# Kernel optimization log

Hardware: AMD Instinct MI355X
Metric: run time of the kernel (lower is better)

The kernel has to match this reference:

```python
import jax, jax.numpy as jnp
import numpy as np

N, B, D, T = 128, 512, 128, 16  # regions, batch, embed_dim, decode steps
C_CLIP = 10.0                   # tanh_clipping
NEG = -1e9


def setup_inputs() -> dict:
    key = jax.random.key(0)
    ks = jax.random.split(key, 40)
    s = 1.0 / np.sqrt(D)

    def w(k, shape):
        return jax.random.uniform(k, shape, jnp.float32, -s, s)

    return {
        'data': jax.random.normal(ks[0], (N, B, 4), jnp.float32),
        'node_embed': w(ks[1], (4, D)),
        'init_placeholder': w(ks[2], (D,)),
        'W1_w': w(ks[3], (D, D)), 'W1_b': w(ks[4], (D,)),
        'W2_w': w(ks[5], (D, D)), 'W2_b': w(ks[6], (D,)),
        'W3_w': w(ks[7], (D, D)), 'W3_b': w(ks[8], (D,)),
        'agg1_w': w(ks[9], (D, D)), 'agg1_b': w(ks[10], (D,)),
        'agg2_w': w(ks[11], (D, D)), 'agg2_b': w(ks[12], (D,)),
        'agg3_w': w(ks[13], (D, D)), 'agg3_b': w(ks[14], (D,)),
        'r1': jnp.ones((1,), jnp.float32),
        'r2': jnp.ones((1,), jnp.float32),
        'r3': jnp.ones((1,), jnp.float32),
        'lstm_Wih': w(ks[15], (4 * D, D)), 'lstm_Whh': w(ks[16], (4 * D, D)),
        'lstm_bih': w(ks[17], (4 * D,)), 'lstm_bhh': w(ks[18], (4 * D,)),
        'ptr_Wq': w(ks[19], (D, D)), 'ptr_bq': w(ks[20], (D,)),
        'ptr_Wref': w(ks[21], (D, D)), 'ptr_bref': w(ks[22], (D,)),
        'ptr_v': w(ks[23], (D,)),
        'glm_Wq': w(ks[24], (D, D)), 'glm_bq': w(ks[25], (D,)),
        'glm_Wref': w(ks[26], (D, D)), 'glm_bref': w(ks[27], (D,)),
        'glm_v': w(ks[28], (D,)),
    }


def _lin(x, w, b):
    return x @ w.T + b


def _attn_logits(q, e, Wq, bq, v):
    # q: [B,D], e: [B,D,N] (1x1-conv-projected ref). Bahdanau: v . tanh(Wq q + e)
    qq = (q @ Wq.T + bq)[:, :, None]          # [B,D,1]
    return jnp.einsum('d,bdn->bn', v, jnp.tanh(qq + e))  # [B,N]


def reference(data, node_embed, init_placeholder,
              W1_w, W1_b, W2_w, W2_b, W3_w, W3_b,
              agg1_w, agg1_b, agg2_w, agg2_b, agg3_w, agg3_b,
              r1, r2, r3,
              lstm_Wih, lstm_Whh, lstm_bih, lstm_bhh,
              ptr_Wq, ptr_bq, ptr_Wref, ptr_bref, ptr_v,
              glm_Wq, glm_bq, glm_Wref, glm_bref, glm_v):
    # node embedding: [N,B,4] @ [4,D] -> [N,B,D]
    emb = jnp.einsum('nbf,fd->nbd', data, node_embed)
    # GPN graph context: gated local transform + aggregated mean over nodes
    ctx = r1 * _lin(emb, W1_w, W1_b) + (1.0 - r1) * jax.nn.relu(_lin(emb.mean(0), agg1_w, agg1_b))
    ctx = r2 * _lin(ctx, W2_w, W2_b) + (1.0 - r2) * jax.nn.relu(_lin(ctx.mean(0), agg2_w, agg2_b))
    ctx = r3 * _lin(ctx, W3_w, W3_b) + (1.0 - r3) * jax.nn.relu(_lin(ctx.mean(0), agg3_w, agg3_b))
    # precompute 1x1-conv ref projections (ref is fixed over decode steps): [B,D,N]
    e_ptr = jnp.einsum('oi,nbi->bon', ptr_Wref, ctx) + ptr_bref[None, :, None]
    e_glm = jnp.einsum('oi,nbi->bon', glm_Wref, ctx) + glm_bref[None, :, None]
    emb_bnd = emb.transpose(1, 0, 2)  # [B,N,D] for gathering next decoder input

    def step(carry, _):
        h, c, x, visited = carry
        # LSTMCell (torch gate order i,f,g,o)
        gates = x @ lstm_Wih.T + lstm_bih + h @ lstm_Whh.T + lstm_bhh
        i, f, g, o = jnp.split(gates, 4, axis=-1)
        c = jax.nn.sigmoid(f) * c + jax.nn.sigmoid(i) * jnp.tanh(g)
        h = jax.nn.sigmoid(o) * jnp.tanh(c)
        # one glimpse (use_tanh=False), masked
        lg = _attn_logits(h, e_glm, glm_Wq, glm_bq, glm_v)
        lg = jnp.where(visited, NEG, lg)
        gl = jnp.einsum('bdn,bn->bd', e_glm, jax.nn.softmax(lg, axis=-1))
        # pointer (use_tanh=True, C=10), masked
        lp = C_CLIP * jnp.tanh(_attn_logits(gl, e_ptr, ptr_Wq, ptr_bq, ptr_v))
        lp = jnp.where(visited, NEG, lp)
        log_p = jax.nn.log_softmax(lp, axis=-1)  # temp = 1.0
        sel = jnp.argmax(log_p, axis=-1)         # greedy decode, [B]
        visited = visited | jax.nn.one_hot(sel, N, dtype=bool)
        x = jnp.take_along_axis(emb_bnd, sel[:, None, None], axis=1)[:, 0]  # [B,D]
        return (h, c, x, visited), log_p

    h0 = jnp.zeros((B, D), emb.dtype)
    c0 = jnp.zeros((B, D), emb.dtype)
    x0 = jnp.broadcast_to(init_placeholder, (B, D)).astype(emb.dtype)
    visited0 = jnp.zeros((B, N), bool)
    _, log_ps = jax.lax.scan(step, (h0, c0, x0, visited0), None, length=T)
    return log_ps  # [T,B,N]
```

## Files before the change

### kernel.cpp

```cpp
#include <hip/hip_runtime.h>
#include <math.h>


#define NREG   128
#define BATCH  512
#define DIM    128
#define TSTEPS 16
#define NEGV   (-1e9f)
#define LOG2E  1.4426950408889634f

__device__ __forceinline__ float fexp2(float x) { return __builtin_amdgcn_exp2f(x); }
__device__ __forceinline__ float frcp(float x)  { return __builtin_amdgcn_rcpf(x); }
__device__ __forceinline__ float fast_tanh(float x) {
    return 1.f - 2.f * frcp(1.f + fexp2(2.8853900817779268f * x));
}
__device__ __forceinline__ float fast_sig(float x) {
    return frcp(1.f + fexp2(-LOG2E * x));
}
__device__ __forceinline__ float fast_exp(float x) { return fexp2(LOG2E * x); }
__device__ __forceinline__ float fast_log(float x) {
    return __builtin_amdgcn_logf(x) * 0.6931471805599453f;
}

__device__ __forceinline__ float dot128(const float* __restrict__ wrow,
                                        const float* __restrict__ s) {
    float a0 = 0.f, a1 = 0.f, a2 = 0.f, a3 = 0.f;
#pragma unroll
    for (int k = 0; k < 128; k += 4) {
        a0 += wrow[k] * s[k];     a1 += wrow[k + 1] * s[k + 1];
        a2 += wrow[k + 2] * s[k + 2]; a3 += wrow[k + 3] * s[k + 3];
    }
    return (a0 + a1) + (a2 + a3);
}

__global__ __launch_bounds__(256) void k_misc(
    const float* __restrict__ Whh, const float* __restrict__ gWq,
    const float* __restrict__ Wih, const float* __restrict__ NE,
    const float* __restrict__ init_ph,
    const float* __restrict__ bih, const float* __restrict__ bhh,
    const float* __restrict__ W1, const float* __restrict__ W2,
    const float* __restrict__ r1p, const float* __restrict__ r2p,
    const float* __restrict__ data,
    float* __restrict__ WhhT, float* __restrict__ gWqT,
    float* __restrict__ WihNE4, float* __restrict__ g0,
    float* __restrict__ bc, float* __restrict__ A21, float* __restrict__ md)
{
    int blk = blockIdx.x, t = threadIdx.x;
    if (blk < 64) {
        int idx = blk * 256 + t;
        int g = idx >> 5, k0 = (idx & 31) * 4;
        float4 v = *(const float4*)(Whh + g * 128 + k0);
        WhhT[(k0 + 0) * 512 + g] = v.x;
        WhhT[(k0 + 1) * 512 + g] = v.y;
        WhhT[(k0 + 2) * 512 + g] = v.z;
        WhhT[(k0 + 3) * 512 + g] = v.w;
    } else if (blk < 80) {
        int idx = (blk - 64) * 256 + t;
        int o = idx >> 5, i0 = (idx & 31) * 4;
        float4 v = *(const float4*)(gWq + o * 128 + i0);
        gWqT[(i0 + 0) * 128 + o] = v.x;
        gWqT[(i0 + 1) * 128 + o] = v.y;
        gWqT[(i0 + 2) * 128 + o] = v.z;
        gWqT[(i0 + 3) * 128 + o] = v.w;
    } else if (blk < 82) {
        int g = (blk - 80) * 256 + t;
        float a0 = 0.f, a1 = 0.f, a2 = 0.f, a3 = 0.f;
        for (int d = 0; d < 128; d += 4) {
            float4 wv = *(const float4*)(Wih + g * 128 + d);
            float4 n0 = *(const float4*)(NE + 0 * 128 + d);
            float4 n1 = *(const float4*)(NE + 1 * 128 + d);
            float4 n2 = *(const float4*)(NE + 2 * 128 + d);
            float4 n3 = *(const float4*)(NE + 3 * 128 + d);
            a0 += wv.x * n0.x + wv.y * n0.y + wv.z * n0.z + wv.w * n0.w;
            a1 += wv.x * n1.x + wv.y * n1.y + wv.z * n1.z + wv.w * n1.w;
            a2 += wv.x * n2.x + wv.y * n2.y + wv.z * n2.z + wv.w * n2.w;
            a3 += wv.x * n3.x + wv.y * n3.y + wv.z * n3.z + wv.w * n3.w;
        }
        *(float4*)(WihNE4 + g * 4) = make_float4(a0, a1, a2, a3);
    } else if (blk == 82) {
        for (int g = t; g < 512; g += 256) {
            float acc = 0.f;
            for (int d = 0; d < 128; d += 4) {
                float4 wv = *(const float4*)(Wih + g * 128 + d);
                float4 iv = *(const float4*)(init_ph + d);
                acc += wv.x * iv.x + wv.y * iv.y + wv.z * iv.z + wv.w * iv.w;
            }
            g0[g] = acc;
            bc[g] = bih[g] + bhh[g];
        }
    } else if (blk < 147) {
        int r = blk - 83;
        int o = r * 2 + (t >> 7), i = t & 127;
        float acc = 0.f;
        for (int k = 0; k < 128; k++) acc += W2[o * 128 + k] * W1[k * 128 + i];
        A21[o * 128 + i] = r1p[0] * r2p[0] * acc;
    } else {
        int idx = (blk - 147) * 256 + t;
        float acc = 0.f;
        for (int n = 0; n < 128; n++) acc += data[n * 2048 + idx];
        md[idx] = acc * (1.f / 128.f);
    }
}

__global__ __launch_bounds__(256) void k_mm2(const float* __restrict__ W3,
                                             const float* __restrict__ A21,
                                             const float* __restrict__ r3p,
                                             float* __restrict__ A3) {
    int o = blockIdx.x * 2 + (threadIdx.x >> 7), i = threadIdx.x & 127;
    float acc = 0.f;
    for (int k = 0; k < 128; k++) acc += W3[o * 128 + k] * A21[k * 128 + i];
    A3[o * 128 + i] = r3p[0] * acc;
}

__global__ __launch_bounds__(256) void k_mm3(const float* __restrict__ gWr,
                                             const float* __restrict__ pWr,
                                             const float* __restrict__ A3,
                                             float* __restrict__ Mg,
                                             float* __restrict__ Mp) {
    int blk = blockIdx.x;
    const float* W = (blk < 64) ? gWr : pWr;
    float* Out = (blk < 64) ? Mg : Mp;
    int r = blk & 63;
    int o = r * 2 + (threadIdx.x >> 7), i = threadIdx.x & 127;
    float acc = 0.f;
    for (int k = 0; k < 128; k++) acc += W[o * 128 + k] * A3[k * 128 + i];
    Out[o * 128 + i] = acc;
}

__global__ __launch_bounds__(256) void k_small2(const float* __restrict__ NE,
                                                const float* __restrict__ Mg,
                                                const float* __restrict__ Mp,
                                                float* __restrict__ Qg4,
                                                float* __restrict__ Qp4) {
    const float* M = (blockIdx.x == 0) ? Mg : Mp;
    float* Q = (blockIdx.x == 0) ? Qg4 : Qp4;
    int t = threadIdx.x;
    for (int idx = t; idx < 512; idx += 256) {
        int o = idx >> 2, f = idx & 3;
        float acc = 0.f;
        for (int d = 0; d < 128; d++) acc += NE[f * 128 + d] * M[o * 128 + d];
        Q[idx] = acc;
    }
}

__global__ __launch_bounds__(256) void k_small3(const float* __restrict__ pWq,
                                                const float* __restrict__ Qg4,
                                                float* __restrict__ GPQ4) {
    int t = threadIdx.x;
    for (int idx = t; idx < 512; idx += 256) {
        int o = idx >> 2, f = idx & 3;
        float acc = 0.f;
        for (int i = 0; i < 128; i++) acc += pWq[o * 128 + i] * Qg4[i * 4 + f];
        GPQ4[idx] = acc;
    }
}

__global__ __launch_bounds__(256) void k_perb(
    const float* __restrict__ md, const float* __restrict__ NE,
    const float* __restrict__ a1w, const float* __restrict__ a1b,
    const float* __restrict__ a2w, const float* __restrict__ a2b,
    const float* __restrict__ a3w, const float* __restrict__ a3b,
    const float* __restrict__ W1, const float* __restrict__ b1,
    const float* __restrict__ W2, const float* __restrict__ b2,
    const float* __restrict__ W3, const float* __restrict__ b3,
    const float* __restrict__ gWr, const float* __restrict__ gbr,
    const float* __restrict__ pWr, const float* __restrict__ pbr,
    const float* __restrict__ pWq, const float* __restrict__ pbq,
    const float* __restrict__ r1p, const float* __restrict__ r2p,
    const float* __restrict__ r3p,
    float* __restrict__ og, float* __restrict__ op, float* __restrict__ pog)
{
    __shared__ float Ws[128 * 129];
    __shared__ float me[1024], Cv[1024], Mv[1024], Tv[1024], C2[1024], M2[1024];
    __shared__ float NEs[512], mdS[32];
    const int t = threadIdx.x;
    const int b0 = blockIdx.x * 8;
    const float r1 = r1p[0], r2 = r2p[0], r3 = r3p[0];

#define STAGE_W(Wptr)                                                          \
    for (int i = t * 4; i < 16384; i += 1024) {                                \
        float4 v = *(const float4*)((Wptr) + i);                               \
        int oo = i >> 7, kk = i & 127;                                         \
        float* p = &Ws[oo * 129 + kk];                                         \
        p[0] = v.x; p[1] = v.y; p[2] = v.z; p[3] = v.w;                        \
    }

    if (t < 32) mdS[t] = md[b0 * 4 + t];
    for (int i = t; i < 512; i += 256) NEs[i] = NE[i];
    __syncthreads();
    for (int idx = t; idx < 1024; idx += 256) {
        int j = idx >> 7, d = idx & 127;
        me[idx] = mdS[j * 4 + 0] * NEs[d] + mdS[j * 4 + 1] * NEs[128 + d] +
                  mdS[j * 4 + 2] * NEs[256 + d] + mdS[j * 4 + 3] * NEs[384 + d];
    }
    STAGE_W(a1w);
    __syncthreads();
    {
        int o = t & 127, jg = t >> 7;
        for (int jj = 0; jj < 4; jj++) {
            int j = jg * 4 + jj;
            float acc = dot128(&Ws[o * 129], &me[j * 128]);
            Tv[j * 128 + o] = (1.f - r1) * fmaxf(acc + a1b[o], 0.f);
        }
    }
    __syncthreads();
    STAGE_W(W1);
    for (int idx = t; idx < 1024; idx += 256) Cv[idx] = r1 * b1[idx & 127] + Tv[idx];
    __syncthreads();
    {
        int o = t & 127, jg = t >> 7;
        for (int jj = 0; jj < 4; jj++) {
            int j = jg * 4 + jj;
            float acc = dot128(&Ws[o * 129], &me[j * 128]);
            Mv[j * 128 + o] = r1 * (acc + b1[o]) + Tv[j * 128 + o];
        }
    }
    __syncthreads();
    STAGE_W(a2w);
    __syncthreads();
    {
        int o = t & 127, jg = t >> 7;
        for (int jj = 0; jj < 4; jj++) {
            int j = jg * 4 + jj;
            float acc = dot128(&Ws[o * 129], &Mv[j * 128]);
            Tv[j * 128 + o] = (1.f - r2) * fmaxf(acc + a2b[o], 0.f);
        }
    }
    __syncthreads();
    STAGE_W(W2);
    __syncthreads();
    {
        int o = t & 127, jg = t >> 7;
        for (int jj = 0; jj < 4; jj++) {
            int j = jg * 4 + jj;
            float ac = dot128(&Ws[o * 129], &Cv[j * 128]);
            float am = dot128(&Ws[o * 129], &Mv[j * 128]);
            C2[j * 128 + o] = r2 * (ac + b2[o]) + Tv[j * 128 + o];
            M2[j * 128 + o] = r2 * (am + b2[o]) + Tv[j * 128 + o];
        }
    }
    __syncthreads();
    STAGE_W(a3w);
    __syncthreads();
    {
        int o = t & 127, jg = t >> 7;
        for (int jj = 0; jj < 4; jj++) {
            int j = jg * 4 + jj;
            float acc = dot128(&Ws[o * 129], &M2[j * 128]);
            Tv[j * 128 + o] = (1.f - r3) * fmaxf(acc + a3b[o], 0.f);
        }
    }
    __syncthreads();
    STAGE_W(W3);
    __syncthreads();
    {
        int o = t & 127, jg = t >> 7;
        for (int jj = 0; jj < 4; jj++) {
            int j = jg * 4 + jj;
            float acc = dot128(&Ws[o * 129], &C2[j * 128]);
            Cv[j * 128 + o] = r3 * (acc + b3[o]) + Tv[j * 128 + o];
        }
    }
    __syncthreads();
    STAGE_W(gWr);
    __syncthreads();
    {
        int o = t & 127, jg = t >> 7;
        for (int jj = 0; jj < 4; jj++) {
            int j = jg * 4 + jj;
            float acc = dot128(&Ws[o * 129], &Cv[j * 128]) + gbr[o];
            Mv[j * 128 + o] = acc;
            og[(long)(b0 + j) * 128 + o] = acc;
        }
    }
    __syncthreads();
    STAGE_W(pWr);
    __syncthreads();
    {
        int o = t & 127, jg = t >> 7;
        for (int jj = 0; jj < 4; jj++) {
            int j = jg * 4 + jj;
            op[(long)(b0 + j) * 128 + o] = dot128(&Ws[o * 129], &Cv[j * 128]) + pbr[o];
        }
    }
    __syncthreads();
    STAGE_W(pWq);
    __syncthreads();
    {
        int o = t & 127, jg = t >> 7;
        for (int jj = 0; jj < 4; jj++) {
            int j = jg * 4 + jj;
            pog[(long)(b0 + j) * 128 + o] = dot128(&Ws[o * 129], &Mv[j * 128]) + pbq[o];
        }
    }
#undef STAGE_W
}

__global__ __launch_bounds__(256, 2) void k_decode(
    const float* __restrict__ dataIn,
    const float* __restrict__ WhhT,
    const float* __restrict__ gWqT,
    const float* __restrict__ WihNE4,
    const float* __restrict__ g0,
    const float* __restrict__ bc,
    const float* __restrict__ Qg4, const float* __restrict__ Qp4,
    const float* __restrict__ GPQ4,
    const float* __restrict__ ogG, const float* __restrict__ opG,
    const float* __restrict__ pogG,
    const float* __restrict__ gbq, const float* __restrict__ vgG,
    const float* __restrict__ vpG,
    float* __restrict__ out)
{
    __shared__ float4 dataS[128];
    __shared__ float4 WihS[512];
    __shared__ float4 QgS[128], QpS[128], GPQS[128];
    __shared__ float g0S[512], bcS[512], gatesS[512];
    __shared__ float ogS[128], opS[128], pogS[128], gbqS[128], vgS[128], vpS[128];
    __shared__ float hS[128], cS[128], qpart[2][128], lpart[2][128], qpS[128];
    __shared__ int visitedS[128];
    __shared__ int selS;

    const int t = threadIdx.x;
    const int b = blockIdx.x;

    if (t < 128) {
        dataS[t] = *(const float4*)(dataIn + ((long)t * 512 + b) * 4);
        QgS[t]  = *(const float4*)(Qg4 + t * 4);
        QpS[t]  = *(const float4*)(Qp4 + t * 4);
        GPQS[t] = *(const float4*)(GPQ4 + t * 4);
        ogS[t]  = ogG[(long)b * 128 + t];
        opS[t]  = opG[(long)b * 128 + t];
        pogS[t] = pogG[(long)b * 128 + t];
        gbqS[t] = gbq[t];
        vgS[t]  = vgG[t];
        vpS[t]  = vpG[t];
        hS[t] = 0.f; cS[t] = 0.f;
        visitedS[t] = 0;
    }
    WihS[t] = *(const float4*)(WihNE4 + t * 4);
    WihS[t + 256] = *(const float4*)(WihNE4 + (t + 256) * 4);
    g0S[t] = g0[t]; g0S[t + 256] = g0[t + 256];
    bcS[t] = bc[t]; bcS[t + 256] = bc[t + 256];
    __syncthreads();

    for (int step = 0; step < TSTEPS; step++) {
        {
            float accA, accB;
            if (step == 0) {
                accA = g0S[2 * t]; accB = g0S[2 * t + 1];
            } else {
                float4 xd = dataS[selS];
                float4 wA = WihS[2 * t], wB = WihS[2 * t + 1];
                accA = xd.x * wA.x + xd.y * wA.y + xd.z * wA.z + xd.w * wA.w;
                accB = xd.x * wB.x + xd.y * wB.y + xd.z * wB.z + xd.w * wB.w;
            }
            accA += bcS[2 * t]; accB += bcS[2 * t + 1];
            const float* w = WhhT + 2 * t;
            float a0 = 0.f, a1 = 0.f, b0_ = 0.f, b1_ = 0.f;
#pragma unroll 8
            for (int k = 0; k < 128; k += 2) {
                float2 w0 = *(const float2*)(w + (long)k * 512);
                float2 w1 = *(const float2*)(w + (long)(k + 1) * 512);
                float h0 = hS[k], h1 = hS[k + 1];
                a0 += w0.x * h0; a1 += w0.y * h0;
                b0_ += w1.x * h1; b1_ += w1.y * h1;
            }
            gatesS[2 * t] = accA + a0 + b0_;
            gatesS[2 * t + 1] = accB + a1 + b1_;
        }
        __syncthreads();
        if (t < 128) {
            float ig = fast_sig(gatesS[t]);
            float fg = fast_sig(gatesS[128 + t]);
            float gg = fast_tanh(gatesS[256 + t]);
            float og_ = fast_sig(gatesS[384 + t]);
            float cn = fg * cS[t] + ig * gg;
            cS[t] = cn;
            hS[t] = og_ * fast_tanh(cn);
        }
        __syncthreads();
        {
            int o = t & 127, h2 = t >> 7;
            const float* w = gWqT + (h2 * 64) * 128 + o;
            float a0 = (h2 == 0) ? gbqS[o] : 0.f, a1 = 0.f;
#pragma unroll 8
            for (int i = 0; i < 64; i += 2) {
                a0 += w[i * 128] * hS[h2 * 64 + i];
                a1 += w[(i + 1) * 128] * hS[h2 * 64 + i + 1];
            }
            qpart[h2][o] = a0 + a1;
        }
        __syncthreads();
        {
            int n = t & 127, h2 = t >> 7;
            float4 dn = dataS[n];
            float acc = 0.f;
#pragma unroll 4
            for (int j = 0; j < 64; j++) {
                int d = h2 * 64 + j;
                float4 qg = QgS[d];
                float eg = dn.x * qg.x + dn.y * qg.y + dn.z * qg.z + dn.w * qg.w
                         + ogS[d];
                float q = qpart[0][d] + qpart[1][d];
                acc += vgS[d] * fast_tanh(q + eg);
            }
            lpart[h2][n] = acc;
        }
        __syncthreads();
        if (t < 64) {
            float l0 = visitedS[t]      ? NEGV : lpart[0][t] + lpart[1][t];
            float l1 = visitedS[t + 64] ? NEGV : lpart[0][t + 64] + lpart[1][t + 64];
            float m = fmaxf(l0, l1);
            for (int off = 32; off; off >>= 1) m = fmaxf(m, __shfl_xor(m, off, 64));
            float p0 = fast_exp(l0 - m), p1 = fast_exp(l1 - m);
            float s = p0 + p1;
            float4 d0 = dataS[t], d1 = dataS[t + 64];
            float q0 = p0 * d0.x + p1 * d1.x;
            float q1 = p0 * d0.y + p1 * d1.y;
            float q2 = p0 * d0.z + p1 * d1.z;
            float q3 = p0 * d0.w + p1 * d1.w;
            for (int off = 32; off; off >>= 1) {
                s  += __shfl_xor(s, off, 64);
                q0 += __shfl_xor(q0, off, 64);
                q1 += __shfl_xor(q1, off, 64);
                q2 += __shfl_xor(q2, off, 64);
                q3 += __shfl_xor(q3, off, 64);
            }
            float inv = frcp(s);
            q0 *= inv; q1 *= inv; q2 *= inv; q3 *= inv;
            float4 gA = GPQS[t];
            qpS[t] = q0 * gA.x + q1 * gA.y + q2 * gA.z + q3 * gA.w + pogS[t];
            float4 gB = GPQS[t + 64];
            qpS[t + 64] = q0 * gB.x + q1 * gB.y + q2 * gB.z + q3 * gB.w + pogS[t + 64];
        }
        __syncthreads();
        {
            int n = t & 127, h2 = t >> 7;
            float4 dn = dataS[n];
            float acc = 0.f;
#pragma unroll 4
            for (int j = 0; j < 64; j++) {
                int d = h2 * 64 + j;
                float4 qp = QpS[d];
                float ep = dn.x * qp.x + dn.y * qp.y + dn.z * qp.z + dn.w * qp.w
                         + opS[d];
                acc += vpS[d] * fast_tanh(qpS[d] + ep);
            }
            lpart[h2][n] = acc;
        }
        __syncthreads();
        if (t < 64) {
            float s0 = lpart[0][t] + lpart[1][t];
            float s1 = lpart[0][t + 64] + lpart[1][t + 64];
            float l0 = visitedS[t]      ? NEGV : 10.f * fast_tanh(s0);
            float l1 = visitedS[t + 64] ? NEGV : 10.f * fast_tanh(s1);
            float m = fmaxf(l0, l1);
            for (int off = 32; off; off >>= 1) m = fmaxf(m, __shfl_xor(m, off, 64));
            float p0 = fast_exp(l0 - m), p1 = fast_exp(l1 - m);
            float s = p0 + p1;
            for (int off = 32; off; off >>= 1) s += __shfl_xor(s, off, 64);
            float lse = m + fast_log(s);
            float* outp = out + ((long)step * BATCH + b) * NREG;
            outp[t] = l0 - lse;
            outp[t + 64] = l1 - lse;
            float v; int idx;
            if (l1 > l0) { v = l1; idx = t + 64; } else { v = l0; idx = t; }
            for (int off = 32; off; off >>= 1) {
                float ov = __shfl_xor(v, off, 64);
                int   oi = __shfl_xor(idx, off, 64);
                if (ov > v || (ov == v && oi < idx)) { v = ov; idx = oi; }
            }
            if (t == 0) { selS = idx; visitedS[idx] = 1; }
        }
        __syncthreads();
    }
}

extern "C" void kernel_launch(void* const* d_in, const int* in_sizes, int n_in,
                              void* d_out, int out_size, void* d_ws, size_t ws_size,
                              hipStream_t stream) {
    const float* data = (const float*)d_in[0];
    const float* NE   = (const float*)d_in[1];
    const float* init = (const float*)d_in[2];
    const float* W1w = (const float*)d_in[3];  const float* W1b = (const float*)d_in[4];
    const float* W2w = (const float*)d_in[5];  const float* W2b = (const float*)d_in[6];
    const float* W3w = (const float*)d_in[7];  const float* W3b = (const float*)d_in[8];
    const float* A1w = (const float*)d_in[9];  const float* A1b = (const float*)d_in[10];
    const float* A2w = (const float*)d_in[11]; const float* A2b = (const float*)d_in[12];
    const float* A3w = (const float*)d_in[13]; const float* A3b = (const float*)d_in[14];
    const float* r1  = (const float*)d_in[15];
    const float* r2  = (const float*)d_in[16];
    const float* r3  = (const float*)d_in[17];
    const float* Wih = (const float*)d_in[18]; const float* Whh = (const float*)d_in[19];
    const float* bih = (const float*)d_in[20]; const float* bhh = (const float*)d_in[21];
    const float* pWq = (const float*)d_in[22]; const float* pbq = (const float*)d_in[23];
    const float* pWr = (const float*)d_in[24]; const float* pbr = (const float*)d_in[25];
    const float* pv  = (const float*)d_in[26];
    const float* gWq = (const float*)d_in[27]; const float* gbq = (const float*)d_in[28];
    const float* gWr = (const float*)d_in[29]; const float* gbr = (const float*)d_in[30];
    const float* gv  = (const float*)d_in[31];
    float* out = (float*)d_out;

    float* ws     = (float*)d_ws;
    float* WhhT   = ws;
    float* gWqT   = WhhT + 65536;
    float* WihNE4 = gWqT + 16384;
    float* g0     = WihNE4 + 2048;
    float* bc     = g0 + 512;
    float* A21    = bc + 512;
    float* A3     = A21 + 16384;
    float* Mg     = A3 + 16384;
    float* Mp     = Mg + 16384;
    float* Qg4    = Mp + 16384;
    float* Qp4    = Qg4 + 512;
    float* GPQ4   = Qp4 + 512;
    float* md     = GPQ4 + 512;
    float* og     = md + 2048;
    float* op     = og + 65536;
    float* pog    = op + 65536;

    k_misc<<<155, 256, 0, stream>>>(Whh, gWq, Wih, NE, init, bih, bhh,
                                    W1w, W2w, r1, r2, data,
                                    WhhT, gWqT, WihNE4, g0, bc, A21, md);
    k_mm2<<<64, 256, 0, stream>>>(W3w, A21, r3, A3);
    k_mm3<<<128, 256, 0, stream>>>(gWr, pWr, A3, Mg, Mp);
    k_small2<<<2, 256, 0, stream>>>(NE, Mg, Mp, Qg4, Qp4);
    k_small3<<<1, 256, 0, stream>>>(pWq, Qg4, GPQ4);
    k_perb<<<64, 256, 0, stream>>>(md, NE, A1w, A1b, A2w, A2b, A3w, A3b,
                                   W1w, W1b, W2w, W2b, W3w, W3b,
                                   gWr, gbr, pWr, pbr, pWq, pbq,
                                   r1, r2, r3, og, op, pog);
    k_decode<<<BATCH, 256, 0, stream>>>(data, WhhT, gWqT, WihNE4, g0, bc,
                                        Qg4, Qp4, GPQ4, og, op, pog,
                                        gbq, gv, pv, out);
}
```

Before: 448.8 us.

## Fuse all precompute kernels into one launch and widen decode to 512 threads

Merges the chain of small setup kernels (the weight-product matmuls, Q projections and per-batch GPN context) into a single multi-role k_misc launch. Block 83 computes the low-rank Q vectors by propagating the node embedding through the weight chain, and the other blocks run the per-batch context including the data mean. Weight transposes become float4-packed layouts. The decode kernel runs with 512 threads, splits the attention reduction four ways, and folds the tanh constant and v-sum into precomputed terms so each logit uses one exp2 and one rcp. This removes several launches and serialized small kernels, at the cost of a more complex kernel with heavy LDS use in one launch.

```diff
diff --git a/kernel.cpp b/kernel.cpp
--- a/kernel.cpp
+++ b/kernel.cpp
@@ -8,11 +8,12 @@
 #define TSTEPS 16
 #define NEGV   (-1e9f)
 #define LOG2E  1.4426950408889634f
+#define CT     2.8853900817779268f
 
 __device__ __forceinline__ float fexp2(float x) { return __builtin_amdgcn_exp2f(x); }
 __device__ __forceinline__ float frcp(float x)  { return __builtin_amdgcn_rcpf(x); }
 __device__ __forceinline__ float fast_tanh(float x) {
-    return 1.f - 2.f * frcp(1.f + fexp2(2.8853900817779268f * x));
+    return 1.f - 2.f * frcp(1.f + fexp2(CT * x));
 }
 __device__ __forceinline__ float fast_sig(float x) {
     return frcp(1.f + fexp2(-LOG2E * x));
@@ -27,7 +28,7 @@
     float a0 = 0.f, a1 = 0.f, a2 = 0.f, a3 = 0.f;
 #pragma unroll
     for (int k = 0; k < 128; k += 4) {
-        a0 += wrow[k] * s[k];     a1 += wrow[k + 1] * s[k + 1];
+        a0 += wrow[k] * s[k];         a1 += wrow[k + 1] * s[k + 1];
         a2 += wrow[k + 2] * s[k + 2]; a3 += wrow[k + 3] * s[k + 3];
     }
     return (a0 + a1) + (a2 + a3);
@@ -38,30 +39,41 @@
     const float* __restrict__ Wih, const float* __restrict__ NE,
     const float* __restrict__ init_ph,
     const float* __restrict__ bih, const float* __restrict__ bhh,
-    const float* __restrict__ W1, const float* __restrict__ W2,
+    const float* __restrict__ W1, const float* __restrict__ b1,
+    const float* __restrict__ W2, const float* __restrict__ b2,
+    const float* __restrict__ W3, const float* __restrict__ b3,
+    const float* __restrict__ a1w, const float* __restrict__ a1b,
+    const float* __restrict__ a2w, const float* __restrict__ a2b,
+    const float* __restrict__ a3w, const float* __restrict__ a3b,
+    const float* __restrict__ gWr, const float* __restrict__ gbr,
+    const float* __restrict__ pWr, const float* __restrict__ pbr,
+    const float* __restrict__ pWq, const float* __restrict__ pbq,
     const float* __restrict__ r1p, const float* __restrict__ r2p,
-    const float* __restrict__ data,
-    float* __restrict__ WhhT, float* __restrict__ gWqT,
+    const float* __restrict__ r3p,
+    const float* __restrict__ pv, const float* __restrict__ data,
+    float* __restrict__ WhhP, float* __restrict__ gWqP,
     float* __restrict__ WihNE4, float* __restrict__ g0,
-    float* __restrict__ bc, float* __restrict__ A21, float* __restrict__ md)
+    float* __restrict__ bc, float* __restrict__ sumvp,
+    float* __restrict__ Qgc, float* __restrict__ Qpc, float* __restrict__ GPQ,
+    float* __restrict__ og, float* __restrict__ op, float* __restrict__ pog)
 {
-    int blk = blockIdx.x, t = threadIdx.x;
+    __shared__ float Ws[128 * 129];
+    __shared__ float me[1024], Cv[1024], Mv[1024], Tv[1024], C2[1024], M2[1024];
+    __shared__ float NEs[512], mdS[32];
+    __shared__ float4 Uc[128], Vc[128], Qgu[128];
+
+    const int blk = blockIdx.x, t = threadIdx.x;
+
     if (blk < 64) {
         int idx = blk * 256 + t;
-        int g = idx >> 5, k0 = (idx & 31) * 4;
-        float4 v = *(const float4*)(Whh + g * 128 + k0);
-        WhhT[(k0 + 0) * 512 + g] = v.x;
-        WhhT[(k0 + 1) * 512 + g] = v.y;
-        WhhT[(k0 + 2) * 512 + g] = v.z;
-        WhhT[(k0 + 3) * 512 + g] = v.w;
+        int kb = idx >> 9, g = idx & 511;
+        float4 v = *(const float4*)(Whh + g * 128 + kb * 4);
+        ((float4*)WhhP)[kb * 512 + g] = v;
     } else if (blk < 80) {
         int idx = (blk - 64) * 256 + t;
-        int o = idx >> 5, i0 = (idx & 31) * 4;
-        float4 v = *(const float4*)(gWq + o * 128 + i0);
-        gWqT[(i0 + 0) * 128 + o] = v.x;
-        gWqT[(i0 + 1) * 128 + o] = v.y;
-        gWqT[(i0 + 2) * 128 + o] = v.z;
-        gWqT[(i0 + 3) * 128 + o] = v.w;
+        int ib = idx >> 7, o = idx & 127;
+        float4 v = *(const float4*)(gWq + o * 128 + ib * 4);
+        ((float4*)gWqP)[ib * 128 + o] = v;
     } else if (blk < 82) {
         int g = (blk - 80) * 256 + t;
         float a0 = 0.f, a1 = 0.f, a2 = 0.f, a3 = 0.f;
@@ -88,337 +100,291 @@
             g0[g] = acc;
             bc[g] = bih[g] + bhh[g];
         }
-    } else if (blk < 147) {
-        int r = blk - 83;
-        int o = r * 2 + (t >> 7), i = t & 127;
-        float acc = 0.f;
-        for (int k = 0; k < 128; k++) acc += W2[o * 128 + k] * W1[k * 128 + i];
-        A21[o * 128 + i] = r1p[0] * r2p[0] * acc;
+        if (t < 64) {
+            float sv = pv[t] + pv[t + 64];
+            for (int off = 32; off; off >>= 1) sv += __shfl_xor(sv, off, 64);
+            if (t == 0) sumvp[0] = sv;
+        }
+    } else if (blk == 83) {
+        if (t < 128)
+            Uc[t] = make_float4(NE[t], NE[128 + t], NE[256 + t], NE[384 + t]);
+        __syncthreads();
+#define CH_STAGE(Wp, SRC, DST, SC)                                             \
+        if (t < 128) {                                                         \
+            const float* wr = (Wp) + t * 128;                                  \
+            float ax = 0.f, ay = 0.f, az = 0.f, aw = 0.f;                      \
+            _Pragma("unroll 8")                                                \
+            for (int k = 0; k < 128; k++) {                                    \
+                float w = wr[k]; float4 u = SRC[k];                            \
+                ax += w * u.x; ay += w * u.y; az += w * u.z; aw += w * u.w;    \
+            }                                                                  \
+            float sc = (SC);                                                   \
+            DST[t] = make_float4(sc * ax, sc * ay, sc * az, sc * aw);          \
+        }                                                                      \
+        __syncthreads();
+        CH_STAGE(W1, Uc, Vc, r1p[0])
+        CH_STAGE(W2, Vc, Uc, r2p[0])
+        CH_STAGE(W3, Uc, Vc, r3p[0])
+        CH_STAGE(gWr, Vc, Qgu, 1.f)
+        CH_STAGE(pWr, Vc, Uc, 1.f)
+        CH_STAGE(pWq, Qgu, Vc, 1.f)
+        if (t < 128) {
+            float4 qg = Qgu[t], qp = Uc[t];
+            ((float4*)Qgc)[t] = make_float4(CT * qg.x, CT * qg.y, CT * qg.z, CT * qg.w);
+            ((float4*)Qpc)[t] = make_float4(CT * qp.x, CT * qp.y, CT * qp.z, CT * qp.w);
+            ((float4*)GPQ)[t] = Vc[t];
+        }
+#undef CH_STAGE
     } else {
-        int idx = (blk - 147) * 256 + t;
-        float acc = 0.f;
-        for (int n = 0; n < 128; n++) acc += data[n * 2048 + idx];
-        md[idx] = acc * (1.f / 128.f);
+        const int b0 = (blk - 84) * 8;
+        const float r1 = r1p[0], r2 = r2p[0], r3 = r3p[0];
+#define STAGE_W(Wptr)                                                          \
+        for (int i = t * 4; i < 16384; i += 1024) {                            \
+            float4 v = *(const float4*)((Wptr) + i);                           \
+            int oo = i >> 7, kk = i & 127;                                     \
+            float* p = &Ws[oo * 129 + kk];                                     \
+            p[0] = v.x; p[1] = v.y; p[2] = v.z; p[3] = v.w;                    \
+        }
+        if (t < 32) {
+            int j = t >> 2, f = t & 3;
+            float acc = 0.f;
+            for (int n = 0; n < 128; n++) acc += data[n * 2048 + (b0 + j) * 4 + f];
+            mdS[t] = acc * (1.f / 128.f);
+        }
+        for (int i = t; i < 512; i += 256) NEs[i] = NE[i];
+        __syncthreads();
+        for (int idx = t; idx < 1024; idx += 256) {
+            int j = idx >> 7, d = idx & 127;
+            me[idx] = mdS[j * 4 + 0] * NEs[d] + mdS[j * 4 + 1] * NEs[128 + d] +
+                      mdS[j * 4 + 2] * NEs[256 + d] + mdS[j * 4 + 3] * NEs[384 + d];
+        }
+        STAGE_W(a1w);
+        __syncthreads();
+        {
+            int o = t & 127, jg = t >> 7;
+            for (int jj = 0; jj < 4; jj++) {
+                int j = jg * 4 + jj;
+                float acc = dot128(&Ws[o * 129], &me[j * 128]);
+                Tv[j * 128 + o] = (1.f - r1) * fmaxf(acc + a1b[o], 0.f);
+            }
+        }
+        __syncthreads();
+        STAGE_W(W1);
+        for (int idx = t; idx < 1024; idx += 256) Cv[idx] = r1 * b1[idx & 127] + Tv[idx];
+        __syncthreads();
+        {
+            int o = t & 127, jg = t >> 7;
+            for (int jj = 0; jj < 4; jj++) {
+                int j = jg * 4 + jj;
+                float acc = dot128(&Ws[o * 129], &me[j * 128]);
+                Mv[j * 128 + o] = r1 * (acc + b1[o]) + Tv[j * 128 + o];
+            }
+        }
+        __syncthreads();
+        STAGE_W(a2w);
+        __syncthreads();
+        {
+            int o = t & 127, jg = t >> 7;
+            for (int jj = 0; jj < 4; jj++) {
+                int j = jg * 4 + jj;
+                float acc = dot128(&Ws[o * 129], &Mv[j * 128]);
+                Tv[j * 128 + o] = (1.f - r2) * fmaxf(acc + a2b[o], 0.f);
+            }
+        }
+        __syncthreads();
+        STAGE_W(W2);
+        __syncthreads();
+        {
+            int o = t & 127, jg = t >> 7;
+            for (int jj = 0; jj < 4; jj++) {
+                int j = jg * 4 + jj;
+                float ac = dot128(&Ws[o * 129], &Cv[j * 128]);
+                float am = dot128(&Ws[o * 129], &Mv[j * 128]);
+                C2[j * 128 + o] = r2 * (ac + b2[o]) + Tv[j * 128 + o];
+                M2[j * 128 + o] = r2 * (am + b2[o]) + Tv[j * 128 + o];
+            }
+        }
+        __syncthreads();
+        STAGE_W(a3w);
+        __syncthreads();
+        {
+            int o = t & 127, jg = t >> 7;
+            for (int jj = 0; jj < 4; jj++) {
+                int j = jg * 4 + jj;
+                float acc = dot128(&Ws[o * 129], &M2[j * 128]);
+                Tv[j * 128 + o] = (1.f - r3) * fmaxf(acc + a3b[o], 0.f);
+            }
+        }
+        __syncthreads();
+        STAGE_W(W3);
+        __syncthreads();
+        {
+            int o = t & 127, jg = t >> 7;
+            for (int jj = 0; jj < 4; jj++) {
+                int j = jg * 4 + jj;
+                float acc = dot128(&Ws[o * 129], &C2[j * 128]);
+                Cv[j * 128 + o] = r3 * (acc + b3[o]) + Tv[j * 128 + o];
+            }
+        }
+        __syncthreads();
+        STAGE_W(gWr);
+        __syncthreads();
+        {
+            int o = t & 127, jg = t >> 7;
+            for (int jj = 0; jj < 4; jj++) {
+                int j = jg * 4 + jj;
+                float acc = dot128(&Ws[o * 129], &Cv[j * 128]) + gbr[o];
+                Mv[j * 128 + o] = acc;
+                og[(long)(b0 + j) * 128 + o] = acc;
+            }
+        }
+        __syncthreads();
+        STAGE_W(pWr);
+        __syncthreads();
+        {
+            int o = t & 127, jg = t >> 7;
+            for (int jj = 0; jj < 4; jj++) {
+                int j = jg * 4 + jj;
+                op[(long)(b0 + j) * 128 + o] = dot128(&Ws[o * 129], &Cv[j * 128]) + pbr[o];
+            }
+        }
+        __syncthreads();
+        STAGE_W(pWq);
+        __syncthreads();
+        {
+            int o = t & 127, jg = t >> 7;
+            for (int jj = 0; jj < 4; jj++) {
+                int j = jg * 4 + jj;
+                pog[(long)(b0 + j) * 128 + o] = dot128(&Ws[o * 129], &Mv[j * 128]) + pbq[o];
+            }
+        }
+#undef STAGE_W
     }
 }
 
-__global__ __launch_bounds__(256) void k_mm2(const float* __restrict__ W3,
-                                             const float* __restrict__ A21,
-                                             const float* __restrict__ r3p,
-                                             float* __restrict__ A3) {
-    int o = blockIdx.x * 2 + (threadIdx.x >> 7), i = threadIdx.x & 127;
-    float acc = 0.f;
-    for (int k = 0; k < 128; k++) acc += W3[o * 128 + k] * A21[k * 128 + i];
-    A3[o * 128 + i] = r3p[0] * acc;
-}
-
-__global__ __launch_bounds__(256) void k_mm3(const float* __restrict__ gWr,
-                                             const float* __restrict__ pWr,
-                                             const float* __restrict__ A3,
-                                             float* __restrict__ Mg,
-                                             float* __restrict__ Mp) {
-    int blk = blockIdx.x;
-    const float* W = (blk < 64) ? gWr : pWr;
-    float* Out = (blk < 64) ? Mg : Mp;
-    int r = blk & 63;
-    int o = r * 2 + (threadIdx.x >> 7), i = threadIdx.x & 127;
-    float acc = 0.f;
-    for (int k = 0; k < 128; k++) acc += W[o * 128 + k] * A3[k * 128 + i];
-    Out[o * 128 + i] = acc;
-}
-
-__global__ __launch_bounds__(256) void k_small2(const float* __restrict__ NE,
-                                                const float* __restrict__ Mg,
-                                                const float* __restrict__ Mp,
-                                                float* __restrict__ Qg4,
-                                                float* __restrict__ Qp4) {
-    const float* M = (blockIdx.x == 0) ? Mg : Mp;
-    float* Q = (blockIdx.x == 0) ? Qg4 : Qp4;
-    int t = threadIdx.x;
-    for (int idx = t; idx < 512; idx += 256) {
-        int o = idx >> 2, f = idx & 3;
-        float acc = 0.f;
-        for (int d = 0; d < 128; d++) acc += NE[f * 128 + d] * M[o * 128 + d];
-        Q[idx] = acc;
-    }
-}
-
-__global__ __launch_bounds__(256) void k_small3(const float* __restrict__ pWq,
-                                                const float* __restrict__ Qg4,
-                                                float* __restrict__ GPQ4) {
-    int t = threadIdx.x;
-    for (int idx = t; idx < 512; idx += 256) {
-        int o = idx >> 2, f = idx & 3;
-        float acc = 0.f;
-        for (int i = 0; i < 128; i++) acc += pWq[o * 128 + i] * Qg4[i * 4 + f];
-        GPQ4[idx] = acc;
-    }
-}
-
-__global__ __launch_bounds__(256) void k_perb(
-    const float* __restrict__ md, const float* __restrict__ NE,
-    const float* __restrict__ a1w, const float* __restrict__ a1b,
-    const float* __restrict__ a2w, const float* __restrict__ a2b,
-    const float* __restrict__ a3w, const float* __restrict__ a3b,
-    const float* __restrict__ W1, const float* __restrict__ b1,
-    const float* __restrict__ W2, const float* __restrict__ b2,
-    const float* __restrict__ W3, const float* __restrict__ b3,
-    const float* __restrict__ gWr, const float* __restrict__ gbr,
-    const float* __restrict__ pWr, const float* __restrict__ pbr,
-    const float* __restrict__ pWq, const float* __restrict__ pbq,
-    const float* __restrict__ r1p, const float* __restrict__ r2p,
-    const float* __restrict__ r3p,
-    float* __restrict__ og, float* __restrict__ op, float* __restrict__ pog)
-{
-    __shared__ float Ws[128 * 129];
-    __shared__ float me[1024], Cv[1024], Mv[1024], Tv[1024], C2[1024], M2[1024];
-    __shared__ float NEs[512], mdS[32];
-    const int t = threadIdx.x;
-    const int b0 = blockIdx.x * 8;
-    const float r1 = r1p[0], r2 = r2p[0], r3 = r3p[0];
-
-#define STAGE_W(Wptr)                                                          \
-    for (int i = t * 4; i < 16384; i += 1024) {                                \
-        float4 v = *(const float4*)((Wptr) + i);                               \
-        int oo = i >> 7, kk = i & 127;                                         \
-        float* p = &Ws[oo * 129 + kk];                                         \
-        p[0] = v.x; p[1] = v.y; p[2] = v.z; p[3] = v.w;                        \
-    }
-
-    if (t < 32) mdS[t] = md[b0 * 4 + t];
-    for (int i = t; i < 512; i += 256) NEs[i] = NE[i];
-    __syncthreads();
-    for (int idx = t; idx < 1024; idx += 256) {
-        int j = idx >> 7, d = idx & 127;
-        me[idx] = mdS[j * 4 + 0] * NEs[d] + mdS[j * 4 + 1] * NEs[128 + d] +
-                  mdS[j * 4 + 2] * NEs[256 + d] + mdS[j * 4 + 3] * NEs[384 + d];
-    }
-    STAGE_W(a1w);
-    __syncthreads();
-    {
-        int o = t & 127, jg = t >> 7;
-        for (int jj = 0; jj < 4; jj++) {
-            int j = jg * 4 + jj;
-            float acc = dot128(&Ws[o * 129], &me[j * 128]);
-            Tv[j * 128 + o] = (1.f - r1) * fmaxf(acc + a1b[o], 0.f);
-        }
-    }
-    __syncthreads();
-    STAGE_W(W1);
-    for (int idx = t; idx < 1024; idx += 256) Cv[idx] = r1 * b1[idx & 127] + Tv[idx];
-    __syncthreads();
-    {
-        int o = t & 127, jg = t >> 7;
-        for (int jj = 0; jj < 4; jj++) {
-            int j = jg * 4 + jj;
-            float acc = dot128(&Ws[o * 129], &me[j * 128]);
-            Mv[j * 128 + o] = r1 * (acc + b1[o]) + Tv[j * 128 + o];
-        }
-    }
-    __syncthreads();
-    STAGE_W(a2w);
-    __syncthreads();
-    {
-        int o = t & 127, jg = t >> 7;
-        for (int jj = 0; jj < 4; jj++) {
-            int j = jg * 4 + jj;
-            float acc = dot128(&Ws[o * 129], &Mv[j * 128]);
-            Tv[j * 128 + o] = (1.f - r2) * fmaxf(acc + a2b[o], 0.f);
-        }
-    }
-    __syncthreads();
-    STAGE_W(W2);
-    __syncthreads();
-    {
-        int o = t & 127, jg = t >> 7;
-        for (int jj = 0; jj < 4; jj++) {
-            int j = jg * 4 + jj;
-            float ac = dot128(&Ws[o * 129], &Cv[j * 128]);
-            float am = dot128(&Ws[o * 129], &Mv[j * 128]);
-            C2[j * 128 + o] = r2 * (ac + b2[o]) + Tv[j * 128 + o];
-            M2[j * 128 + o] = r2 * (am + b2[o]) + Tv[j * 128 + o];
-        }
-    }
-    __syncthreads();
-    STAGE_W(a3w);
-    __syncthreads();
-    {
-        int o = t & 127, jg = t >> 7;
-        for (int jj = 0; jj < 4; jj++) {
-            int j = jg * 4 + jj;
-            float acc = dot128(&Ws[o * 129], &M2[j * 128]);
-            Tv[j * 128 + o] = (1.f - r3) * fmaxf(acc + a3b[o], 0.f);
-        }
-    }
-    __syncthreads();
-    STAGE_W(W3);
-    __syncthreads();
-    {
-        int o = t & 127, jg = t >> 7;
-        for (int jj = 0; jj < 4; jj++) {
-            int j = jg * 4 + jj;
-            float acc = dot128(&Ws[o * 129], &C2[j * 128]);
-            Cv[j * 128 + o] = r3 * (acc + b3[o]) + Tv[j * 128 + o];
-        }
-    }
-    __syncthreads();
-    STAGE_W(gWr);
-    __syncthreads();
-    {
-        int o = t & 127, jg = t >> 7;
-        for (int jj = 0; jj < 4; jj++) {
-            int j = jg * 4 + jj;
-            float acc = dot128(&Ws[o * 129], &Cv[j * 128]) + gbr[o];
-            Mv[j * 128 + o] = acc;
-            og[(long)(b0 + j) * 128 + o] = acc;
-        }
-    }
-    __syncthreads();
-    STAGE_W(pWr);
-    __syncthreads();
-    {
-        int o = t & 127, jg = t >> 7;
-        for (int jj = 0; jj < 4; jj++) {
-            int j = jg * 4 + jj;
-            op[(long)(b0 + j) * 128 + o] = dot128(&Ws[o * 129], &Cv[j * 128]) + pbr[o];
-        }
-    }
-    __syncthreads();
-    STAGE_W(pWq);
-    __syncthreads();
-    {
-        int o = t & 127, jg = t >> 7;
-        for (int jj = 0; jj < 4; jj++) {
-            int j = jg * 4 + jj;
-            pog[(long)(b0 + j) * 128 + o] = dot128(&Ws[o * 129], &Mv[j * 128]) + pbq[o];
-        }
-    }
-#undef STAGE_W
-}
-
-__global__ __launch_bounds__(256, 2) void k_decode(
+__global__ __launch_bounds__(512, 4) void k_decode(
     const float* __restrict__ dataIn,
-    const float* __restrict__ WhhT,
-    const float* __restrict__ gWqT,
+    const float* __restrict__ WhhP,
+    const float* __restrict__ gWqP,
     const float* __restrict__ WihNE4,
     const float* __restrict__ g0,
     const float* __restrict__ bc,
-    const float* __restrict__ Qg4, const float* __restrict__ Qp4,
-    const float* __restrict__ GPQ4,
+    const float* __restrict__ Qgc, const float* __restrict__ Qpc,
+    const float* __restrict__ GPQ,
     const float* __restrict__ ogG, const float* __restrict__ opG,
     const float* __restrict__ pogG,
     const float* __restrict__ gbq, const float* __restrict__ vgG,
-    const float* __restrict__ vpG,
+    const float* __restrict__ vpG, const float* __restrict__ sumvpG,
     float* __restrict__ out)
 {
     __shared__ float4 dataS[128];
     __shared__ float4 WihS[512];
-    __shared__ float4 QgS[128], QpS[128], GPQS[128];
+    __shared__ float4 QgcS[128], QpcS[128], GPQS[128];
     __shared__ float g0S[512], bcS[512], gatesS[512];
-    __shared__ float ogS[128], opS[128], pogS[128], gbqS[128], vgS[128], vpS[128];
-    __shared__ float hS[128], cS[128], qpart[2][128], lpart[2][128], qpS[128];
-    __shared__ int visitedS[128];
-    __shared__ int selS;
+    __shared__ float ogS[128], opS[128], pogS[128];
+    __shared__ float gbqS[128], vg2S[128], vp2S[128];
+    __shared__ float hS[128], cS[128], qeS[128], qepS[128];
+    __shared__ float lpart[4][128];
+    __shared__ int   visitedS[128];
+    __shared__ int   selS;
+    __shared__ float sumvpS;
 
     const int t = threadIdx.x;
     const int b = blockIdx.x;
 
     if (t < 128) {
         dataS[t] = *(const float4*)(dataIn + ((long)t * 512 + b) * 4);
-        QgS[t]  = *(const float4*)(Qg4 + t * 4);
-        QpS[t]  = *(const float4*)(Qp4 + t * 4);
-        GPQS[t] = *(const float4*)(GPQ4 + t * 4);
-        ogS[t]  = ogG[(long)b * 128 + t];
-        opS[t]  = opG[(long)b * 128 + t];
-        pogS[t] = pogG[(long)b * 128 + t];
-        gbqS[t] = gbq[t];
-        vgS[t]  = vgG[t];
-        vpS[t]  = vpG[t];
+        QgcS[t]  = ((const float4*)Qgc)[t];
+        QpcS[t]  = ((const float4*)Qpc)[t];
+        GPQS[t]  = ((const float4*)GPQ)[t];
+        ogS[t]   = ogG[(long)b * 128 + t];
+        opS[t]   = opG[(long)b * 128 + t];
+        pogS[t]  = pogG[(long)b * 128 + t];
+        gbqS[t]  = gbq[t];
+        vg2S[t]  = -2.f * vgG[t];
+        vp2S[t]  = -2.f * vpG[t];
         hS[t] = 0.f; cS[t] = 0.f;
         visitedS[t] = 0;
     }
-    WihS[t] = *(const float4*)(WihNE4 + t * 4);
-    WihS[t + 256] = *(const float4*)(WihNE4 + (t + 256) * 4);
-    g0S[t] = g0[t]; g0S[t + 256] = g0[t + 256];
-    bcS[t] = bc[t]; bcS[t + 256] = bc[t + 256];
+    WihS[t] = ((const float4*)WihNE4)[t];
+    g0S[t] = g0[t];
+    bcS[t] = bc[t];
+    if (t == 0) sumvpS = sumvpG[0];
     __syncthreads();
 
     for (int step = 0; step < TSTEPS; step++) {
         {
-            float accA, accB;
+            float ihp;
             if (step == 0) {
-                accA = g0S[2 * t]; accB = g0S[2 * t + 1];
+                ihp = g0S[t];
             } else {
                 float4 xd = dataS[selS];
-                float4 wA = WihS[2 * t], wB = WihS[2 * t + 1];
-                accA = xd.x * wA.x + xd.y * wA.y + xd.z * wA.z + xd.w * wA.w;
-                accB = xd.x * wB.x + xd.y * wB.y + xd.z * wB.z + xd.w * wB.w;
-            }
-            accA += bcS[2 * t]; accB += bcS[2 * t + 1];
-            const float* w = WhhT + 2 * t;
-            float a0 = 0.f, a1 = 0.f, b0_ = 0.f, b1_ = 0.f;
+                float4 w = WihS[t];
+                ihp = xd.x * w.x + xd.y * w.y + xd.z * w.z + xd.w * w.w;
+            }
+            ihp += bcS[t];
+            const float4* wp = (const float4*)WhhP + t;
+            float a0 = 0.f, a1 = 0.f, a2 = 0.f, a3 = 0.f;
 #pragma unroll 8
-            for (int k = 0; k < 128; k += 2) {
-                float2 w0 = *(const float2*)(w + (long)k * 512);
-                float2 w1 = *(const float2*)(w + (long)(k + 1) * 512);
-                float h0 = hS[k], h1 = hS[k + 1];
-                a0 += w0.x * h0; a1 += w0.y * h0;
-                b0_ += w1.x * h1; b1_ += w1.y * h1;
-            }
-            gatesS[2 * t] = accA + a0 + b0_;
-            gatesS[2 * t + 1] = accB + a1 + b1_;
+            for (int kb = 0; kb < 32; kb++) {
+                float4 w = wp[kb * 512];
+                a0 += w.x * hS[4 * kb];     a1 += w.y * hS[4 * kb + 1];
+                a2 += w.z * hS[4 * kb + 2]; a3 += w.w * hS[4 * kb + 3];
+            }
+            gatesS[t] = ihp + (a0 + a1) + (a2 + a3);
         }
         __syncthreads();
         if (t < 128) {
-            float ig = fast_sig(gatesS[t]);
-            float fg = fast_sig(gatesS[128 + t]);
-            float gg = fast_tanh(gatesS[256 + t]);
+            float ig  = fast_sig(gatesS[t]);
+            float fg  = fast_sig(gatesS[128 + t]);
+            float gg  = fast_tanh(gatesS[256 + t]);
             float og_ = fast_sig(gatesS[384 + t]);
             float cn = fg * cS[t] + ig * gg;
             cS[t] = cn;
             hS[t] = og_ * fast_tanh(cn);
         }
         __syncthreads();
-        {
-            int o = t & 127, h2 = t >> 7;
-            const float* w = gWqT + (h2 * 64) * 128 + o;
-            float a0 = (h2 == 0) ? gbqS[o] : 0.f, a1 = 0.f;
+        if (t < 128) {
+            const float4* wp = (const float4*)gWqP + t;
+            float a0 = 0.f, a1 = 0.f, a2 = 0.f, a3 = 0.f;
 #pragma unroll 8
-            for (int i = 0; i < 64; i += 2) {
-                a0 += w[i * 128] * hS[h2 * 64 + i];
-                a1 += w[(i + 1) * 128] * hS[h2 * 64 + i + 1];
-            }
-            qpart[h2][o] = a0 + a1;
-        }
-        __syncthreads();
-        {
-            int n = t & 127, h2 = t >> 7;
+            for (int ib = 0; ib < 32; ib++) {
+                float4 w = wp[ib * 128];
+                a0 += w.x * hS[4 * ib];     a1 += w.y * hS[4 * ib + 1];
+                a2 += w.z * hS[4 * ib + 2]; a3 += w.w * hS[4 * ib + 3];
+            }
+            float q = (a0 + a1) + (a2 + a3) + gbqS[t];
+            qeS[t] = CT * (q + ogS[t]);
+        }
+        __syncthreads();
+        {
+            int n = t & 127, q4 = t >> 7, d0 = q4 * 32;
             float4 dn = dataS[n];
             float acc = 0.f;
-#pragma unroll 4
-            for (int j = 0; j < 64; j++) {
-                int d = h2 * 64 + j;
-                float4 qg = QgS[d];
-                float eg = dn.x * qg.x + dn.y * qg.y + dn.z * qg.z + dn.w * qg.w
-                         + ogS[d];
-                float q = qpart[0][d] + qpart[1][d];
-                acc += vgS[d] * fast_tanh(q + eg);
-            }
-            lpart[h2][n] = acc;
+#pragma unroll 8
+            for (int j = 0; j < 32; j++) {
+                int d = d0 + j;
+                float4 qg = QgcS[d];
+                float x = qeS[d] + dn.x * qg.x + dn.y * qg.y + dn.z * qg.z + dn.w * qg.w;
+                acc += vg2S[d] * frcp(1.f + fexp2(x));
+            }
+            lpart[q4][n] = acc;
         }
         __syncthreads();
         if (t < 64) {
-            float l0 = visitedS[t]      ? NEGV : lpart[0][t] + lpart[1][t];
-            float l1 = visitedS[t + 64] ? NEGV : lpart[0][t + 64] + lpart[1][t + 64];
+            float l0 = visitedS[t] ? NEGV
+                     : (lpart[0][t] + lpart[1][t]) + (lpart[2][t] + lpart[3][t]);
+            float l1 = visitedS[t + 64] ? NEGV
+                     : (lpart[0][t + 64] + lpart[1][t + 64]) + (lpart[2][t + 64] + lpart[3][t + 64]);
             float m = fmaxf(l0, l1);
             for (int off = 32; off; off >>= 1) m = fmaxf(m, __shfl_xor(m, off, 64));
             float p0 = fast_exp(l0 - m), p1 = fast_exp(l1 - m);
             float s = p0 + p1;
-            float4 d0 = dataS[t], d1 = dataS[t + 64];
-            float q0 = p0 * d0.x + p1 * d1.x;
-            float q1 = p0 * d0.y + p1 * d1.y;
-            float q2 = p0 * d0.z + p1 * d1.z;
-            float q3 = p0 * d0.w + p1 * d1.w;
+            float4 d0v = dataS[t], d1v = dataS[t + 64];
+            float q0 = p0 * d0v.x + p1 * d1v.x;
+            float q1 = p0 * d0v.y + p1 * d1v.y;
+            float q2 = p0 * d0v.z + p1 * d1v.z;
+            float q3 = p0 * d0v.w + p1 * d1v.w;
             for (int off = 32; off; off >>= 1) {
                 s  += __shfl_xor(s, off, 64);
                 q0 += __shfl_xor(q0, off, 64);
@@ -429,29 +395,31 @@
             float inv = frcp(s);
             q0 *= inv; q1 *= inv; q2 *= inv; q3 *= inv;
             float4 gA = GPQS[t];
-            qpS[t] = q0 * gA.x + q1 * gA.y + q2 * gA.z + q3 * gA.w + pogS[t];
+            qepS[t] = CT * (q0 * gA.x + q1 * gA.y + q2 * gA.z + q3 * gA.w
+                            + pogS[t] + opS[t]);
             float4 gB = GPQS[t + 64];
-            qpS[t + 64] = q0 * gB.x + q1 * gB.y + q2 * gB.z + q3 * gB.w + pogS[t + 64];
-        }
-        __syncthreads();
-        {
-            int n = t & 127, h2 = t >> 7;
+            qepS[t + 64] = CT * (q0 * gB.x + q1 * gB.y + q2 * gB.z + q3 * gB.w
+                                 + pogS[t + 64] + opS[t + 64]);
+        }
+        __syncthreads();
+        {
+            int n = t & 127, q4 = t >> 7, d0 = q4 * 32;
             float4 dn = dataS[n];
             float acc = 0.f;
-#pragma unroll 4
-            for (int j = 0; j < 64; j++) {
-                int d = h2 * 64 + j;
-                float4 qp = QpS[d];
-                float ep = dn.x * qp.x + dn.y * qp.y + dn.z * qp.z + dn.w * qp.w
-                         + opS[d];
-                acc += vpS[d] * fast_tanh(qpS[d] + ep);
-            }
-            lpart[h2][n] = acc;
+#pragma unroll 8
+            for (int j = 0; j < 32; j++) {
+                int d = d0 + j;
+                float4 qp = QpcS[d];
+                float x = qepS[d] + dn.x * qp.x + dn.y * qp.y + dn.z * qp.z + dn.w * qp.w;
+                acc += vp2S[d] * frcp(1.f + fexp2(x));
+            }
+            lpart[q4][n] = acc;
         }
         __syncthreads();
         if (t < 64) {
-            float s0 = lpart[0][t] + lpart[1][t];
-            float s1 = lpart[0][t + 64] + lpart[1][t + 64];
+            float s0 = sumvpS + (lpart[0][t] + lpart[1][t]) + (lpart[2][t] + lpart[3][t]);
+            float s1 = sumvpS + (lpart[0][t + 64] + lpart[1][t + 64])
+                              + (lpart[2][t + 64] + lpart[3][t + 64]);
             float l0 = visitedS[t]      ? NEGV : 10.f * fast_tanh(s0);
             float l1 = visitedS[t + 64] ? NEGV : 10.f * fast_tanh(s1);
             float m = fmaxf(l0, l1);
@@ -502,35 +470,27 @@
     float* out = (float*)d_out;
 
     float* ws     = (float*)d_ws;
-    float* WhhT   = ws;
-    float* gWqT   = WhhT + 65536;
-    float* WihNE4 = gWqT + 16384;
+    float* WhhP   = ws;
+    float* gWqP   = WhhP + 65536;
+    float* WihNE4 = gWqP + 16384;
     float* g0     = WihNE4 + 2048;
     float* bc     = g0 + 512;
-    float* A21    = bc + 512;
-    float* A3     = A21 + 16384;
-    float* Mg     = A3 + 16384;
-    float* Mp     = Mg + 16384;
-    float* Qg4    = Mp + 16384;
-    float* Qp4    = Qg4 + 512;
-    float* GPQ4   = Qp4 + 512;
-    float* md     = GPQ4 + 512;
-    float* og     = md + 2048;
+    float* Qgc    = bc + 512;
+    float* Qpc    = Qgc + 512;
+    float* GPQ    = Qpc + 512;
+    float* og     = GPQ + 512;
     float* op     = og + 65536;
     float* pog    = op + 65536;
-
-    k_misc<<<155, 256, 0, stream>>>(Whh, gWq, Wih, NE, init, bih, bhh,
-                                    W1w, W2w, r1, r2, data,
-                                    WhhT, gWqT, WihNE4, g0, bc, A21, md);
-    k_mm2<<<64, 256, 0, stream>>>(W3w, A21, r3, A3);
-    k_mm3<<<128, 256, 0, stream>>>(gWr, pWr, A3, Mg, Mp);
-    k_small2<<<2, 256, 0, stream>>>(NE, Mg, Mp, Qg4, Qp4);
-    k_small3<<<1, 256, 0, stream>>>(pWq, Qg4, GPQ4);
-    k_perb<<<64, 256, 0, stream>>>(md, NE, A1w, A1b, A2w, A2b, A3w, A3b,
-                                   W1w, W1b, W2w, W2b, W3w, W3b,
-                                   gWr, gbr, pWr, pbr, pWq, pbq,
-                                   r1, r2, r3, og, op, pog);
-    k_decode<<<BATCH, 256, 0, stream>>>(data, WhhT, gWqT, WihNE4, g0, bc,
-                                        Qg4, Qp4, GPQ4, og, op, pog,
-                                        gbq, gv, pv, out);
-}
+    float* sumvp  = pog + 65536;
+
+    k_misc<<<148, 256, 0, stream>>>(Whh, gWq, Wih, NE, init, bih, bhh,
+                                    W1w, W1b, W2w, W2b, W3w, W3b,
+                                    A1w, A1b, A2w, A2b, A3w, A3b,
+                                    gWr, gbr, pWr, pbr, pWq, pbq,
+                                    r1, r2, r3, pv, data,
+                                    WhhP, gWqP, WihNE4, g0, bc, sumvp,
+                                    Qgc, Qpc, GPQ, og, op, pog);
+    k_decode<<<BATCH, 512, 0, stream>>>(data, WhhP, gWqP, WihNE4, g0, bc,
+                                        Qgc, Qpc, GPQ, og, op, pog,
+                                        gbq, gv, pv, sumvp, out);
+}
```

Result: faster. 366.5 us (median of 3 runs) (-18.3%).
